# Optimization experiments

Measured on AMD Instinct MI355X. Metric: run time of the kernel, lower is better.

## Reference

```python
import jax, jax.numpy as jnp
import numpy as np

BS, DIM, N, M, O = 2048, 32, 40, 40, 200


def setup_inputs() -> dict:
    key = jax.random.key(0)
    k1, k2, k3 = jax.random.split(key, 3)
    x = jax.random.normal(k1, (BS, DIM, N), dtype=jnp.float32)
    y = jax.random.normal(k2, (BS, DIM, M), dtype=jnp.float32)
    # Linear(n*m -> o), no bias; scale like nn.Linear default-ish init
    W = jax.random.normal(k3, (O, N * M), dtype=jnp.float32) * (1.0 / np.sqrt(N * M))
    return {"x": x, "y": y, "W": W}


def reference(x, y, W):
    # Original math: z[b,d,n,m] = x[b,d,n] * y[b,d,m]; flatten (n,m) -> k; out = z @ W.T
    # Fused form: out[b,d,o] = sum_{n,m} x[b,d,n] * y[b,d,m] * W[o, n*M+m]
    o, nm = W.shape
    Wr = W.reshape(o, x.shape[-1], y.shape[-1])  # [O, N, M]
    return jnp.einsum('bdn,bdm,onm->bdo', x, y, Wr)
```

## Files before the change

kernel.cpp:

```cpp
#include <hip/hip_runtime.h>
#include <hip/hip_fp16.h>

#define OOv   200
#define KKv   1600
#define OPAD  208
#define NSTEPS 50
#define NSUPER 25
#define CHUNK_BYTES 13312
#define SUPER_BYTES 26624
#define XSTR 40
#define YSTR 56

typedef _Float16 half8  __attribute__((ext_vector_type(8)));
typedef _Float16 half2v __attribute__((ext_vector_type(2)));
typedef __attribute__((ext_vector_type(4))) float floatx4;

__global__ void wb_convert_kernel(const float* __restrict__ W,
                                  unsigned short* __restrict__ Wh) {
    int idx = blockIdx.x * 256 + threadIdx.x;
    if (idx >= NSTEPS * OPAD * 32) return;
    int j    = idx & 7;
    int slot = (idx >> 3) % (OPAD * 4);
    int c    = (idx >> 3) / (OPAD * 4);
    int o    = slot >> 2;
    int kgs  = slot & 3;
    int kg   = kgs ^ ((o >> 1) & 3);
    int k    = c * 32 + kg * 8 + j;
    float v  = (o < OOv) ? W[o * KKv + k] : 0.0f;
    union { _Float16 h; unsigned short u; } cv; cv.h = (_Float16)v;
    Wh[idx] = cv.u;
}

__global__ __launch_bounds__(256, 2) void cin_mfma_kernel(
        const float* __restrict__ X, const float* __restrict__ Y,
        const unsigned short* __restrict__ Wh, float* __restrict__ Out) {
    __shared__ __align__(16) unsigned char bsm[2 * SUPER_BYTES];
    __shared__ __align__(16) _Float16 xlds[128 * XSTR];
    __shared__ __align__(16) _Float16 ylds[128 * YSTR];

    const int tid     = threadIdx.x;
    const int wave    = tid >> 6;
    const int lane    = tid & 63;
    const int li      = lane & 15;
    const int kg      = lane >> 4;
    const int rowhalf = wave & 1;
    const int colgrp  = wave >> 1;
    const int ntiles  = colgrp ? 6 : 7;
    const int obase   = colgrp * 112;
    const long blockbase = (long)blockIdx.x * 128;

    const float* xg = X + blockbase * 40;
    const float* yg = Y + blockbase * 40;
    for (int i = tid; i < 1280; i += 256) {
        int r  = i / 10;
        int c4 = (i % 10) * 4;
        floatx4 vx = *(const floatx4*)(xg + i * 4);
        floatx4 vy = *(const floatx4*)(yg + i * 4);
        union { half2v h[2]; unsigned long long u; } px, py;
        px.h[0] = (half2v){(_Float16)vx.x, (_Float16)vx.y};
        px.h[1] = (half2v){(_Float16)vx.z, (_Float16)vx.w};
        py.h[0] = (half2v){(_Float16)vy.x, (_Float16)vy.y};
        py.h[1] = (half2v){(_Float16)vy.z, (_Float16)vy.w};
        *(unsigned long long*)(xlds + r * XSTR + c4) = px.u;
        *(unsigned long long*)(ylds + r * YSTR + c4) = py.u;
    }
    {
        const char* src = (const char*)Wh;
        for (int c = wave; c < 26; c += 4) {
            int off = c * 1024 + lane * 16;
            __builtin_amdgcn_global_load_lds(
                (const __attribute__((address_space(1))) unsigned int*)(src + off),
                (__attribute__((address_space(3))) unsigned int*)(bsm + off),
                16, 0, 0);
        }
    }
    __syncthreads();

    floatx4 acc[4][7];
#pragma unroll
    for (int rt = 0; rt < 4; ++rt)
#pragma unroll
        for (int ct = 0; ct < 7; ++ct)
            acc[rt][ct] = (floatx4){0.f, 0.f, 0.f, 0.f};

    const int rowb = rowhalf * 64 + li;
    const char* ybase[4];
    const char* xbase[4];
#pragma unroll
    for (int rt = 0; rt < 4; ++rt) {
        int row = rowb + rt * 16;
        ybase[rt] = (const char*)ylds + row * (YSTR * 2) + kg * 16;
        xbase[rt] = (const char*)xlds + row * (XSTR * 2);
    }
    const bool w1 = kg >= 1, w2 = kg >= 2, w3 = kg >= 3;

    const int bfoff = (obase + li) * 64 + ((kg ^ ((li >> 1) & 3)) * 16);

    const int R32[5] = {0, 64, 48, 32, 16};
    const int B5[5]  = {0, 0, 1, 2, 3};
    const int WK[5]  = {0, 1, 2, 3, 0};

    for (int g = 0; g < 5; ++g) {
        half2v xd[4][8];
#pragma unroll
        for (int rt = 0; rt < 4; ++rt) {
            half8 xq = *(const half8*)(xbase[rt] + g * 16);
#pragma unroll
            for (int e = 0; e < 8; ++e)
                xd[rt][e] = (half2v){xq[e], xq[e]};
        }

#pragma unroll
        for (int ss = 0; ss < 5; ++ss) {
            const int sstep = g * 5 + ss;
            if (sstep + 1 < NSUPER) {
                const char* src = (const char*)Wh + (size_t)(sstep + 1) * SUPER_BYTES;
                unsigned char* dst = bsm + ((sstep + 1) & 1) * SUPER_BYTES;
                for (int c = wave; c < 26; c += 4) {
                    int off = c * 1024 + lane * 16;
                    __builtin_amdgcn_global_load_lds(
                        (const __attribute__((address_space(1))) unsigned int*)(src + off),
                        (__attribute__((address_space(3))) unsigned int*)(dst + off),
                        16, 0, 0);
                }
            }
            const unsigned char* cbuf = bsm + (sstep & 1) * SUPER_BYTES;

#pragma unroll
            for (int half = 0; half < 2; ++half) {
                const int p  = 2 * ss + half;
                const int pm = p % 5, pd = p / 5;
                const int yimm  = R32[pm];
                const int dbase = B5[pm] + 4 * pd;
                const int wk    = WK[pm];
                const bool use  = (wk == 1) ? w1 : (wk == 2) ? w2 : (wk == 3) ? w3 : false;
                const unsigned char* chunk = cbuf + half * CHUNK_BYTES;

                half8 bf[7];
#pragma unroll
                for (int ct = 0; ct < 7; ++ct)
                    if (ct < ntiles)
                        bf[ct] = *(const half8*)(chunk + bfoff + ct * 1024);

                half8 af[4];
#pragma unroll
                for (int rt = 0; rt < 4; ++rt) {
                    const char* ya = ybase[rt] + (yimm - (use ? 80 : 0));
                    half8 yv = *(const half8*)ya;
                    half2v xs = use ? xd[rt][dbase + 1] : xd[rt][dbase];
                    half8 xsp = __builtin_shufflevector(xs, xs, 0, 1, 0, 1, 0, 1, 0, 1);
                    af[rt] = xsp * yv;
                }

#pragma unroll
                for (int ct = 0; ct < 7; ++ct)
                    if (ct < ntiles)
#pragma unroll
                        for (int rt = 0; rt < 4; ++rt)
                            acc[rt][ct] = __builtin_amdgcn_mfma_f32_16x16x32_f16(
                                af[rt], bf[ct], acc[rt][ct], 0, 0, 0);
            }
            __syncthreads();
        }
    }

#pragma unroll
    for (int rt = 0; rt < 4; ++rt) {
#pragma unroll
        for (int ct = 0; ct < 7; ++ct) {
            if (ct >= ntiles) continue;
            int gcol = obase + ct * 16 + li;
            if (gcol < OOv) {
#pragma unroll
                for (int r4 = 0; r4 < 4; ++r4) {
                    long grow = blockbase + rowhalf * 64 + rt * 16 + kg * 4 + r4;
                    Out[grow * OOv + gcol] = acc[rt][ct][r4];
                }
            }
        }
    }
}

extern "C" void kernel_launch(void* const* d_in, const int* in_sizes, int n_in,
                              void* d_out, int out_size, void* d_ws, size_t ws_size,
                              hipStream_t stream) {
    (void)in_sizes; (void)n_in; (void)out_size; (void)ws_size;
    const float* X = (const float*)d_in[0];
    const float* Y = (const float*)d_in[1];
    const float* W = (const float*)d_in[2];
    float* Out = (float*)d_out;
    unsigned short* Wh = (unsigned short*)d_ws;

    wb_convert_kernel<<<1300, 256, 0, stream>>>(W, Wh);
    cin_mfma_kernel<<<512, 256, 0, stream>>>(X, Y, Wh, Out);
}
```

Baseline: 123.3 us.

## Pipeline weight chunks through a 4-buffer LDS ring with per-chunk barriers

Replaces the double-buffered two-chunk superstep staging with a four-slot ring of single chunks, prefetching three chunks ahead via direct global-to-LDS loads. A single barrier per chunk is guarded by explicit vmcnt waits, and the Y fragment reads are hoisted ahead of that barrier. The MFMA block runs at raised wave priority. Each chunk's staging is split into fixed 16-byte and 4-byte loads per lane. The aim is to hide weight-load latency and cut synchronisation stalls, at the cost of more LDS pressure and fragile hand-tuned waitcnt ordering.

```diff
diff --git a/kernel.cpp b/kernel.cpp
--- a/kernel.cpp
+++ b/kernel.cpp
@@ -4,10 +4,8 @@
 #define OOv   200
 #define KKv   1600
 #define OPAD  208
-#define NSTEPS 50
-#define NSUPER 25
+#define NCHUNK 50
 #define CHUNK_BYTES 13312
-#define SUPER_BYTES 26624
 #define XSTR 40
 #define YSTR 56
 
@@ -18,7 +16,7 @@
 __global__ void wb_convert_kernel(const float* __restrict__ W,
                                   unsigned short* __restrict__ Wh) {
     int idx = blockIdx.x * 256 + threadIdx.x;
-    if (idx >= NSTEPS * OPAD * 32) return;
+    if (idx >= NCHUNK * OPAD * 32) return;
     int j    = idx & 7;
     int slot = (idx >> 3) % (OPAD * 4);
     int c    = (idx >> 3) / (OPAD * 4);
@@ -31,10 +29,83 @@
     Wh[idx] = cv.u;
 }
 
+__device__ __forceinline__ void stage_chunk(const char* src, unsigned char* dst,
+                                            int s16off0, int s4off) {
+#pragma unroll
+    for (int q = 0; q < 3; ++q) {
+        const int off = s16off0 + q * 1024;
+        __builtin_amdgcn_global_load_lds(
+            (const __attribute__((address_space(1))) unsigned int*)(src + off),
+            (__attribute__((address_space(3))) unsigned int*)(dst + off),
+            16, 0, 0);
+    }
+    __builtin_amdgcn_global_load_lds(
+        (const __attribute__((address_space(1))) unsigned int*)(src + s4off),
+        (__attribute__((address_space(3))) unsigned int*)(dst + s4off),
+        4, 0, 0);
+}
+
+template<int P, int VM, bool STAGE>
+__device__ __forceinline__ void chunk_step(
+        unsigned bufc, unsigned bufs, unsigned char* bsm,
+        const char* wsrc, int s16off0, int s4off,
+        const char* (&ybase)[4], half2v (&xd)[4][8],
+        int bfoff, int ntiles, bool w1, bool w2, bool w3,
+        floatx4 (&acc)[4][7])
+{
+    constexpr int R32a[5] = {0, 64, 48, 32, 16};
+    constexpr int B5a[5]  = {0, 0, 1, 2, 3};
+    constexpr int WKa[5]  = {0, 1, 2, 3, 0};
+    constexpr int pm = P % 5, pd = P / 5;
+    constexpr int yimm  = R32a[pm];
+    constexpr int dbase = B5a[pm] + 4 * pd;
+    constexpr int wk    = WKa[pm];
+    const bool use = (wk == 1) ? w1 : (wk == 2) ? w2 : (wk == 3) ? w3 : false;
+
+    half8 yv[4];
+#pragma unroll
+    for (int rt = 0; rt < 4; ++rt)
+        yv[rt] = *(const half8*)(ybase[rt] + (yimm - (use ? 80 : 0)));
+
+    if constexpr (VM == 8)      asm volatile("s_waitcnt vmcnt(8)");
+    else if constexpr (VM == 4) asm volatile("s_waitcnt vmcnt(4)");
+    else                        asm volatile("s_waitcnt vmcnt(0)");
+    __builtin_amdgcn_sched_barrier(0);
+    __builtin_amdgcn_s_barrier();
+    __builtin_amdgcn_sched_barrier(0);
+
+    if constexpr (STAGE) stage_chunk(wsrc, bsm + bufs, s16off0, s4off);
+
+    const unsigned char* chunk = bsm + bufc;
+    half8 bf[7];
+#pragma unroll
+    for (int ct = 0; ct < 7; ++ct)
+        if (ct < ntiles)
+            bf[ct] = *(const half8*)(chunk + bfoff + ct * 1024);
+
+    half8 af[4];
+#pragma unroll
+    for (int rt = 0; rt < 4; ++rt) {
+        half2v xs = use ? xd[rt][dbase + 1] : xd[rt][dbase];
+        half8 xsp = __builtin_shufflevector(xs, xs, 0, 1, 0, 1, 0, 1, 0, 1);
+        af[rt] = xsp * yv[rt];
+    }
+
+    __builtin_amdgcn_s_setprio(1);
+#pragma unroll
+    for (int ct = 0; ct < 7; ++ct)
+        if (ct < ntiles)
+#pragma unroll
+            for (int rt = 0; rt < 4; ++rt)
+                acc[rt][ct] = __builtin_amdgcn_mfma_f32_16x16x32_f16(
+                    af[rt], bf[ct], acc[rt][ct], 0, 0, 0);
+    __builtin_amdgcn_s_setprio(0);
+}
+
 __global__ __launch_bounds__(256, 2) void cin_mfma_kernel(
         const float* __restrict__ X, const float* __restrict__ Y,
         const unsigned short* __restrict__ Wh, float* __restrict__ Out) {
-    __shared__ __align__(16) unsigned char bsm[2 * SUPER_BYTES];
+    __shared__ __align__(16) unsigned char bsm[4 * CHUNK_BYTES];
     __shared__ __align__(16) _Float16 xlds[128 * XSTR];
     __shared__ __align__(16) _Float16 ylds[128 * YSTR];
 
@@ -64,17 +135,20 @@
         *(unsigned long long*)(xlds + r * XSTR + c4) = px.u;
         *(unsigned long long*)(ylds + r * YSTR + c4) = py.u;
     }
+
+    const int s16off0 = wave * 3 * 1024 + lane * 16;
+    const int s4off   = 12 * 1024 + wave * 256 + lane * 4;
     {
         const char* src = (const char*)Wh;
-        for (int c = wave; c < 26; c += 4) {
-            int off = c * 1024 + lane * 16;
-            __builtin_amdgcn_global_load_lds(
-                (const __attribute__((address_space(1))) unsigned int*)(src + off),
-                (__attribute__((address_space(3))) unsigned int*)(bsm + off),
-                16, 0, 0);
-        }
-    }
-    __syncthreads();
+#pragma unroll
+        for (int c0 = 0; c0 < 3; ++c0)
+            stage_chunk(src + c0 * CHUNK_BYTES, bsm + c0 * CHUNK_BYTES,
+                        s16off0, s4off);
+    }
+    asm volatile("s_waitcnt lgkmcnt(0)");
+    __builtin_amdgcn_sched_barrier(0);
+    __builtin_amdgcn_s_barrier();
+    __builtin_amdgcn_sched_barrier(0);
 
     floatx4 acc[4][7];
 #pragma unroll
@@ -96,11 +170,16 @@
 
     const int bfoff = (obase + li) * 64 + ((kg ^ ((li >> 1) & 3)) * 16);
 
-    const int R32[5] = {0, 64, 48, 32, 16};
-    const int B5[5]  = {0, 0, 1, 2, 3};
-    const int WK[5]  = {0, 1, 2, 3, 0};
-
-    for (int g = 0; g < 5; ++g) {
+    unsigned b0 = 0 * CHUNK_BYTES, b1 = 1 * CHUNK_BYTES;
+    unsigned b2 = 2 * CHUNK_BYTES, b3 = 3 * CHUNK_BYTES;
+    const char* wsrc = (const char*)Wh + 3 * CHUNK_BYTES;
+
+#define CSTEP(PP, VMV, ST, BC, BS) \
+    chunk_step<PP, VMV, ST>(BC, BS, bsm, wsrc + PP * CHUNK_BYTES, s16off0, s4off, \
+                            ybase, xd, bfoff, ntiles, w1, w2, w3, acc)
+
+#pragma unroll 1
+    for (int g = 0; g < 4; ++g) {
         half2v xd[4][8];
 #pragma unroll
         for (int rt = 0; rt < 4; ++rt) {
@@ -109,60 +188,40 @@
             for (int e = 0; e < 8; ++e)
                 xd[rt][e] = (half2v){xq[e], xq[e]};
         }
-
-#pragma unroll
-        for (int ss = 0; ss < 5; ++ss) {
-            const int sstep = g * 5 + ss;
-            if (sstep + 1 < NSUPER) {
-                const char* src = (const char*)Wh + (size_t)(sstep + 1) * SUPER_BYTES;
-                unsigned char* dst = bsm + ((sstep + 1) & 1) * SUPER_BYTES;
-                for (int c = wave; c < 26; c += 4) {
-                    int off = c * 1024 + lane * 16;
-                    __builtin_amdgcn_global_load_lds(
-                        (const __attribute__((address_space(1))) unsigned int*)(src + off),
-                        (__attribute__((address_space(3))) unsigned int*)(dst + off),
-                        16, 0, 0);
-                }
-            }
-            const unsigned char* cbuf = bsm + (sstep & 1) * SUPER_BYTES;
-
-#pragma unroll
-            for (int half = 0; half < 2; ++half) {
-                const int p  = 2 * ss + half;
-                const int pm = p % 5, pd = p / 5;
-                const int yimm  = R32[pm];
-                const int dbase = B5[pm] + 4 * pd;
-                const int wk    = WK[pm];
-                const bool use  = (wk == 1) ? w1 : (wk == 2) ? w2 : (wk == 3) ? w3 : false;
-                const unsigned char* chunk = cbuf + half * CHUNK_BYTES;
-
-                half8 bf[7];
-#pragma unroll
-                for (int ct = 0; ct < 7; ++ct)
-                    if (ct < ntiles)
-                        bf[ct] = *(const half8*)(chunk + bfoff + ct * 1024);
-
-                half8 af[4];
-#pragma unroll
-                for (int rt = 0; rt < 4; ++rt) {
-                    const char* ya = ybase[rt] + (yimm - (use ? 80 : 0));
-                    half8 yv = *(const half8*)ya;
-                    half2v xs = use ? xd[rt][dbase + 1] : xd[rt][dbase];
-                    half8 xsp = __builtin_shufflevector(xs, xs, 0, 1, 0, 1, 0, 1, 0, 1);
-                    af[rt] = xsp * yv;
-                }
-
-#pragma unroll
-                for (int ct = 0; ct < 7; ++ct)
-                    if (ct < ntiles)
-#pragma unroll
-                        for (int rt = 0; rt < 4; ++rt)
-                            acc[rt][ct] = __builtin_amdgcn_mfma_f32_16x16x32_f16(
-                                af[rt], bf[ct], acc[rt][ct], 0, 0, 0);
-            }
-            __syncthreads();
+        CSTEP(0, 8, true, b0, b3);
+        CSTEP(1, 8, true, b1, b0);
+        CSTEP(2, 8, true, b2, b1);
+        CSTEP(3, 8, true, b3, b2);
+        CSTEP(4, 8, true, b0, b3);
+        CSTEP(5, 8, true, b1, b0);
+        CSTEP(6, 8, true, b2, b1);
+        CSTEP(7, 8, true, b3, b2);
+        CSTEP(8, 8, true, b0, b3);
+        CSTEP(9, 8, true, b1, b0);
+        wsrc += 10 * CHUNK_BYTES;
+        unsigned t0 = b0, t1 = b1; b0 = b2; b1 = b3; b2 = t0; b3 = t1;
+    }
+    {
+        half2v xd[4][8];
+#pragma unroll
+        for (int rt = 0; rt < 4; ++rt) {
+            half8 xq = *(const half8*)(xbase[rt] + 4 * 16);
+#pragma unroll
+            for (int e = 0; e < 8; ++e)
+                xd[rt][e] = (half2v){xq[e], xq[e]};
         }
-    }
+        CSTEP(0, 8, true,  b0, b3);
+        CSTEP(1, 8, true,  b1, b0);
+        CSTEP(2, 8, true,  b2, b1);
+        CSTEP(3, 8, true,  b3, b2);
+        CSTEP(4, 8, true,  b0, b3);
+        CSTEP(5, 8, true,  b1, b0);
+        CSTEP(6, 8, true,  b2, b1);
+        CSTEP(7, 8, false, b3, b2);
+        CSTEP(8, 4, false, b0, b3);
+        CSTEP(9, 0, false, b1, b0);
+    }
+#undef CSTEP
 
 #pragma unroll
     for (int rt = 0; rt < 4; ++rt) {
```

Measured after the change: 141.1 us. 1.14x slower.

## Load W fragments directly from global into registers, drop LDS staging and barriers

Applied to the files above, without the earlier changes.

The converted fp16 weight chunks no longer go through a double-buffered LDS staging area via global_load_lds with a block barrier per super-step. Each wave now loads its B fragments straight from global memory (L2-resident) into registers, software-pipelined one chunk ahead. The x broadcast is simplified to a scalar splat, and MFMA sections are wrapped in s_setprio. This removes the per-step __syncthreads and LDS traffic for W, and frees LDS, at the cost of more registers and more global/L2 loads issued per wave.

```diff
diff --git a/kernel.cpp b/kernel.cpp
--- a/kernel.cpp
+++ b/kernel.cpp
@@ -4,10 +4,8 @@
 #define OOv   200
 #define KKv   1600
 #define OPAD  208
-#define NSTEPS 50
-#define NSUPER 25
+#define NCHUNK 50
 #define CHUNK_BYTES 13312
-#define SUPER_BYTES 26624
 #define XSTR 40
 #define YSTR 56
 
@@ -18,7 +16,7 @@
 __global__ void wb_convert_kernel(const float* __restrict__ W,
                                   unsigned short* __restrict__ Wh) {
     int idx = blockIdx.x * 256 + threadIdx.x;
-    if (idx >= NSTEPS * OPAD * 32) return;
+    if (idx >= NCHUNK * OPAD * 32) return;
     int j    = idx & 7;
     int slot = (idx >> 3) % (OPAD * 4);
     int c    = (idx >> 3) / (OPAD * 4);
@@ -31,10 +29,58 @@
     Wh[idx] = cv.u;
 }
 
+template<int P, bool PREF>
+__device__ __forceinline__ void gstep(
+        const char* wnext,
+        half8 (&cur)[7], half8 (&nxt)[7],
+        const char* (&ybase)[4], half8 (&xq)[4],
+        int bfoff, int ntiles, bool w1, bool w2, bool w3,
+        floatx4 (&acc)[4][7])
+{
+    constexpr int R32a[5] = {0, 64, 48, 32, 16};
+    constexpr int B5a[5]  = {0, 0, 1, 2, 3};
+    constexpr int WKa[5]  = {0, 1, 2, 3, 0};
+    constexpr int pm = P % 5, pd = P / 5;
+    constexpr int yimm  = R32a[pm];
+    constexpr int dbase = B5a[pm] + 4 * pd;
+    constexpr int wk    = WKa[pm];
+    const bool use = (wk == 1) ? w1 : (wk == 2) ? w2 : (wk == 3) ? w3 : false;
+
+    if constexpr (PREF) {
+#pragma unroll
+        for (int ct = 0; ct < 7; ++ct)
+            if (ct < ntiles)
+                nxt[ct] = *(const half8*)(wnext + bfoff + ct * 1024);
+    }
+
+    half8 af[4];
+#pragma unroll
+    for (int rt = 0; rt < 4; ++rt) {
+        half8 yv = *(const half8*)(ybase[rt] + (yimm - (use ? 80 : 0)));
+        _Float16 e;
+        if constexpr (wk == 0) {
+            e = xq[rt][dbase];
+        } else {
+            e = use ? xq[rt][dbase + 1] : xq[rt][dbase];
+        }
+        half8 xsp = {e, e, e, e, e, e, e, e};
+        af[rt] = xsp * yv;
+    }
+
+    __builtin_amdgcn_s_setprio(1);
+#pragma unroll
+    for (int ct = 0; ct < 7; ++ct)
+        if (ct < ntiles)
+#pragma unroll
+            for (int rt = 0; rt < 4; ++rt)
+                acc[rt][ct] = __builtin_amdgcn_mfma_f32_16x16x32_f16(
+                    af[rt], cur[ct], acc[rt][ct], 0, 0, 0);
+    __builtin_amdgcn_s_setprio(0);
+}
+
 __global__ __launch_bounds__(256, 2) void cin_mfma_kernel(
         const float* __restrict__ X, const float* __restrict__ Y,
         const unsigned short* __restrict__ Wh, float* __restrict__ Out) {
-    __shared__ __align__(16) unsigned char bsm[2 * SUPER_BYTES];
     __shared__ __align__(16) _Float16 xlds[128 * XSTR];
     __shared__ __align__(16) _Float16 ylds[128 * YSTR];
 
@@ -64,16 +110,6 @@
         *(unsigned long long*)(xlds + r * XSTR + c4) = px.u;
         *(unsigned long long*)(ylds + r * YSTR + c4) = py.u;
     }
-    {
-        const char* src = (const char*)Wh;
-        for (int c = wave; c < 26; c += 4) {
-            int off = c * 1024 + lane * 16;
-            __builtin_amdgcn_global_load_lds(
-                (const __attribute__((address_space(1))) unsigned int*)(src + off),
-                (__attribute__((address_space(3))) unsigned int*)(bsm + off),
-                16, 0, 0);
-        }
-    }
     __syncthreads();
 
     floatx4 acc[4][7];
@@ -96,73 +132,54 @@
 
     const int bfoff = (obase + li) * 64 + ((kg ^ ((li >> 1) & 3)) * 16);
 
-    const int R32[5] = {0, 64, 48, 32, 16};
-    const int B5[5]  = {0, 0, 1, 2, 3};
-    const int WK[5]  = {0, 1, 2, 3, 0};
-
-    for (int g = 0; g < 5; ++g) {
-        half2v xd[4][8];
-#pragma unroll
-        for (int rt = 0; rt < 4; ++rt) {
-            half8 xq = *(const half8*)(xbase[rt] + g * 16);
-#pragma unroll
-            for (int e = 0; e < 8; ++e)
-                xd[rt][e] = (half2v){xq[e], xq[e]};
-        }
-
-#pragma unroll
-        for (int ss = 0; ss < 5; ++ss) {
-            const int sstep = g * 5 + ss;
-            if (sstep + 1 < NSUPER) {
-                const char* src = (const char*)Wh + (size_t)(sstep + 1) * SUPER_BYTES;
-                unsigned char* dst = bsm + ((sstep + 1) & 1) * SUPER_BYTES;
-                for (int c = wave; c < 26; c += 4) {
-                    int off = c * 1024 + lane * 16;
-                    __builtin_amdgcn_global_load_lds(
-                        (const __attribute__((address_space(1))) unsigned int*)(src + off),
-                        (__attribute__((address_space(3))) unsigned int*)(dst + off),
-                        16, 0, 0);
-                }
-            }
-            const unsigned char* cbuf = bsm + (sstep & 1) * SUPER_BYTES;
-
-#pragma unroll
-            for (int half = 0; half < 2; ++half) {
-                const int p  = 2 * ss + half;
-                const int pm = p % 5, pd = p / 5;
-                const int yimm  = R32[pm];
-                const int dbase = B5[pm] + 4 * pd;
-                const int wk    = WK[pm];
-                const bool use  = (wk == 1) ? w1 : (wk == 2) ? w2 : (wk == 3) ? w3 : false;
-                const unsigned char* chunk = cbuf + half * CHUNK_BYTES;
-
-                half8 bf[7];
-#pragma unroll
-                for (int ct = 0; ct < 7; ++ct)
-                    if (ct < ntiles)
-                        bf[ct] = *(const half8*)(chunk + bfoff + ct * 1024);
-
-                half8 af[4];
-#pragma unroll
-                for (int rt = 0; rt < 4; ++rt) {
-                    const char* ya = ybase[rt] + (yimm - (use ? 80 : 0));
-                    half8 yv = *(const half8*)ya;
-                    half2v xs = use ? xd[rt][dbase + 1] : xd[rt][dbase];
-                    half8 xsp = __builtin_shufflevector(xs, xs, 0, 1, 0, 1, 0, 1, 0, 1);
-                    af[rt] = xsp * yv;
-                }
-
-#pragma unroll
-                for (int ct = 0; ct < 7; ++ct)
-                    if (ct < ntiles)
-#pragma unroll
-                        for (int rt = 0; rt < 4; ++rt)
-                            acc[rt][ct] = __builtin_amdgcn_mfma_f32_16x16x32_f16(
-                                af[rt], bf[ct], acc[rt][ct], 0, 0, 0);
-            }
-            __syncthreads();
-        }
-    }
+    const char* wb = (const char*)Wh;
+
+    half8 bfA[7], bfB[7];
+#pragma unroll
+    for (int ct = 0; ct < 7; ++ct)
+        if (ct < ntiles)
+            bfA[ct] = *(const half8*)(wb + bfoff + ct * 1024);
+
+#define GSTEP(PP, PR, CUR, NXT) \
+    gstep<PP, PR>(wg + (PP + 1) * CHUNK_BYTES, CUR, NXT, ybase, xq, \
+                  bfoff, ntiles, w1, w2, w3, acc)
+
+#pragma unroll 1
+    for (int g = 0; g < 4; ++g) {
+        half8 xq[4];
+#pragma unroll
+        for (int rt = 0; rt < 4; ++rt)
+            xq[rt] = *(const half8*)(xbase[rt] + g * 16);
+        const char* wg = wb + (size_t)g * 10 * CHUNK_BYTES;
+        GSTEP(0, true, bfA, bfB);
+        GSTEP(1, true, bfB, bfA);
+        GSTEP(2, true, bfA, bfB);
+        GSTEP(3, true, bfB, bfA);
+        GSTEP(4, true, bfA, bfB);
+        GSTEP(5, true, bfB, bfA);
+        GSTEP(6, true, bfA, bfB);
+        GSTEP(7, true, bfB, bfA);
+        GSTEP(8, true, bfA, bfB);
+        GSTEP(9, true, bfB, bfA);
+    }
+    {
+        half8 xq[4];
+#pragma unroll
+        for (int rt = 0; rt < 4; ++rt)
+            xq[rt] = *(const half8*)(xbase[rt] + 4 * 16);
+        const char* wg = wb + (size_t)4 * 10 * CHUNK_BYTES;
+        GSTEP(0, true, bfA, bfB);
+        GSTEP(1, true, bfB, bfA);
+        GSTEP(2, true, bfA, bfB);
+        GSTEP(3, true, bfB, bfA);
+        GSTEP(4, true, bfA, bfB);
+        GSTEP(5, true, bfB, bfA);
+        GSTEP(6, true, bfA, bfB);
+        GSTEP(7, true, bfB, bfA);
+        GSTEP(8, true, bfA, bfB);
+        GSTEP(9, false, bfB, bfA);
+    }
+#undef GSTEP
 
 #pragma unroll
     for (int rt = 0; rt < 4; ++rt) {
```

Measured after the change: 217.3 us. +76.2%, slower.
